# Performance work log

Measured on AMD Instinct MI355X. Metric: run time of the kernel, lower is better.

The kernel has to match this reference:

```python
import jax, jax.numpy as jnp
import numpy as np

B, D, H, W, N = 64, 512, 32, 32, 20
E = 512  # emb_size
TEMP = 10.0


def setup_inputs() -> dict:
    key = jax.random.key(0)
    ks = jax.random.split(key, 16)
    inp = {
        "fvisu": jax.random.normal(ks[0], (B, D, H, W), jnp.float32),
        "fword": jax.random.normal(ks[1], (B, N, D), jnp.float32),
        "context_score": jax.random.uniform(ks[2], (B, N), jnp.float32),
        "fcoord": jax.random.normal(ks[3], (B, 8, H, W), jnp.float32),
        "gest": jax.random.normal(ks[4], (B, 8), jnp.float32),
        "word_mask": jax.random.randint(ks[5], (B, N), 0, 2, jnp.int32),
        # parameters (kaiming-uniform-ish scale)
        "attn_map_w": jax.random.normal(ks[6], (E // 2, D), jnp.float32) * (1.0 / np.sqrt(D)),
        "attn_map_b": jnp.zeros((E // 2,), jnp.float32),
        "attn_score_w": jax.random.normal(ks[7], (1, E // 2), jnp.float32) * (1.0 / np.sqrt(E // 2)),
        "attn_score_b": jnp.zeros((1,), jnp.float32),
        "gamma_w": jax.random.normal(ks[8], (2 * E, D), jnp.float32) * (1.0 / np.sqrt(D)),
        "gamma_b": jnp.zeros((2 * E,), jnp.float32),
        "conv1_w": jax.random.normal(ks[9], (E, D + 8), jnp.float32) * (1.0 / np.sqrt(D + 8)),
        "conv1_b": jnp.zeros((E,), jnp.float32),
    }
    return inp


def mask_softmax(attn_score, word_mask, temp=TEMP):
    # score: (B, N)
    score = jax.nn.softmax(attn_score * temp, axis=1)
    m = word_mask.astype(jnp.int32)
    m = m.at[:, 0].set(0)                      # zero CLS position
    idx = jnp.sum(m, axis=1)                   # index of SEP (post-CLS-zeroing), matches torch loop
    m = m.at[jnp.arange(m.shape[0]), idx].set(0)
    ms = score * m.astype(score.dtype)
    return ms / (jnp.sum(ms, axis=1, keepdims=True) + 1e-8)


def reference(fvisu, fword, context_score, fcoord, gest, word_mask,
              attn_map_w, attn_map_b, attn_score_w, attn_score_b,
              gamma_w, gamma_b, conv1_w, conv1_b):
    # fword: (B, N, D) -> module permutes to (B, D, N)
    fw = jnp.transpose(fword, (0, 2, 1))                      # (B, D, N)
    tile_visu = jnp.mean(fvisu.reshape(B, D, -1), axis=2, keepdims=True)  # (B, D, 1)
    context_tile = tile_visu * fw * context_score[:, None, :]  # (B, D, N)

    # 1x1 Conv1d -> GEMM
    attn_feat = jnp.tanh(jnp.einsum('od,bdn->bon', attn_map_w, context_tile)
                         + attn_map_b[None, :, None])          # (B, E/2, N)
    attn_score = (jnp.einsum('oc,bcn->bon', attn_score_w, attn_feat)[:, 0, :]
                  + attn_score_b[0])                           # (B, N)

    mask_score = mask_softmax(attn_score, word_mask)            # (B, N)
    attn_lang = jnp.einsum('bn,bnd->bd', mask_score, fword)     # (B, D)

    # FiLM parameter decode
    film = attn_lang @ gamma_w.T + gamma_b                      # (B, 2E)
    gammas = jnp.tanh(film[:, :E])[:, :, None, None]
    betas = jnp.tanh(film[:, E:])[:, :, None, None]

    # 1x1 Conv2d on concat(fvisu, fcoord) + InstanceNorm2d (no affine, eps=1e-5)
    x = jnp.concatenate([fvisu, fcoord], axis=1)                # (B, D+8, H, W)
    conv = jnp.einsum('oc,bchw->bohw', conv1_w, x) + conv1_b[None, :, None, None]
    mu = jnp.mean(conv, axis=(2, 3), keepdims=True)
    var = jnp.var(conv, axis=(2, 3), keepdims=True)
    norm = (conv - mu) * jax.lax.rsqrt(var + 1e-5)

    fmodu = jax.nn.relu(gammas * norm + betas)
    fmodu = fvisu + fmodu
    return fmodu, attn_lang, attn_score
```

## Files before the change

kernel.cpp:

```cpp
#include <hip/hip_runtime.h>
#include <math.h>

#define BB 64
#define DD 512
#define HW 1024
#define NN 20
#define EE 512
#define CIN 520
#define KCN 17
#define TEMP_F 10.0f

#define OUT_ALANG (BB*DD*HW)
#define OUT_ASCORE (OUT_ALANG + BB*DD)

typedef __bf16 bf16x8 __attribute__((ext_vector_type(8)));
typedef float f32x4 __attribute__((ext_vector_type(4)));

__device__ __forceinline__ unsigned int pack2bf(float a, float b) {
    unsigned int ua = __builtin_bit_cast(unsigned int, a);
    unsigned int ub = __builtin_bit_cast(unsigned int, b);
    ua += 0x7fffu + ((ua >> 16) & 1u);
    ub += 0x7fffu + ((ub >> 16) & 1u);
    return (ua >> 16) | (ub & 0xffff0000u);
}

__device__ __forceinline__ unsigned short bfr(float x) {
    unsigned int u = __builtin_bit_cast(unsigned int, x);
    u += 0x7fffu + ((u >> 16) & 1u);
    return (unsigned short)(u >> 16);
}

__device__ __forceinline__ float bf2f(unsigned short u) {
    unsigned int x = ((unsigned int)u) << 16;
    return __builtin_bit_cast(float, x);
}

__device__ __forceinline__ void glds16(const void* g, void* l) {
    __builtin_amdgcn_global_load_lds(
        (const __attribute__((address_space(1))) void*)g,
        (__attribute__((address_space(3))) void*)l, 16, 0, 0);
}

__global__ __launch_bounds__(256) void k_tilevisu(const float* __restrict__ fvisu,
                                                  float* __restrict__ tv) {
    int row = blockIdx.x;
    const float4* p = (const float4*)(fvisu + (size_t)row * HW);
    int tid = threadIdx.x;
    float4 v = p[tid];
    float s = v.x + v.y + v.z + v.w;
    #pragma unroll
    for (int off = 32; off; off >>= 1) s += __shfl_down(s, off, 64);
    __shared__ float part[4];
    if ((tid & 63) == 0) part[tid >> 6] = s;
    __syncthreads();
    if (tid == 0) tv[row] = (part[0] + part[1] + part[2] + part[3]) * (1.0f / HW);
}

__global__ __launch_bounds__(512) void k_convert_x(
    const float* __restrict__ fvisu, const float* __restrict__ fcoord,
    unsigned short* __restrict__ Xf, float* __restrict__ tv) {
    int L = blockIdx.x;
    int kc = L % KCN;
    int b  = L / KCN;
    int t = threadIdx.x;
    int co = t >> 7;
    int tl = t & 127;
    int cbase = kc * 32 + co * 8;
    float sums[8];
    #pragma unroll
    for (int j = 0; j < 8; ++j) sums[j] = 0.f;

    #pragma unroll
    for (int i = 0; i < 2; ++i) {
        int p0 = (tl + 128 * i) * 4;
        float4 f4[8];
        #pragma unroll
        for (int j = 0; j < 8; ++j) {
            int c = cbase + j;
            if (c < DD) {
                f4[j] = *(const float4*)&fvisu[((size_t)b * DD + c) * HW + p0];
            } else if (c < CIN) {
                f4[j] = *(const float4*)&fcoord[((size_t)b * 8 + (c - DD)) * HW + p0];
            } else {
                f4[j] = make_float4(0.f, 0.f, 0.f, 0.f);
            }
        }
        #pragma unroll
        for (int j = 0; j < 8; ++j)
            if (cbase + j < DD) sums[j] += f4[j].x + f4[j].y + f4[j].z + f4[j].w;

        size_t base = (((size_t)b * 64 + (p0 >> 4)) * KCN + kc) * 512
                    + (size_t)(co * 16 + (p0 & 15)) * 8;
        #pragma unroll
        for (int i2 = 0; i2 < 4; ++i2) {
            uint4 v;
            v.x = pack2bf(((const float*)&f4[0])[i2], ((const float*)&f4[1])[i2]);
            v.y = pack2bf(((const float*)&f4[2])[i2], ((const float*)&f4[3])[i2]);
            v.z = pack2bf(((const float*)&f4[4])[i2], ((const float*)&f4[5])[i2]);
            v.w = pack2bf(((const float*)&f4[6])[i2], ((const float*)&f4[7])[i2]);
            *(uint4*)&Xf[base + (size_t)i2 * 8] = v;
        }
    }

    #pragma unroll
    for (int j = 0; j < 8; ++j) {
        float s = sums[j];
        #pragma unroll
        for (int off = 32; off; off >>= 1) s += __shfl_down(s, off, 64);
        sums[j] = s;
    }
    __shared__ float red[8][8];
    int w = t >> 6;
    if ((t & 63) == 0) {
        #pragma unroll
        for (int j = 0; j < 8; ++j) red[w][j] = sums[j];
    }
    __syncthreads();
    if (t < 32) {
        int j = t & 7, c2 = t >> 3;
        int c = kc * 32 + c2 * 8 + j;
        if (c < DD) tv[(size_t)b * DD + c] = (red[c2 * 2][j] + red[c2 * 2 + 1][j]) * (1.0f / HW);
    }
}

__global__ __launch_bounds__(256) void k_convert_w(
    const float* __restrict__ cw, unsigned short* __restrict__ Wf) {
    int t = threadIdx.x;
    int frag = blockIdx.x * 4 + (t >> 6);
    int l = t & 63;
    int M = frag / KCN, kc = frag % KCN;
    int o = M * 16 + (l & 15);
    int k0 = kc * 32 + (l >> 4) * 8;
    float f[8];
    #pragma unroll
    for (int j = 0; j < 8; ++j) {
        int k = k0 + j;
        f[j] = (k < CIN) ? cw[(size_t)o * CIN + k] : 0.f;
    }
    uint4 v;
    v.x = pack2bf(f[0], f[1]);
    v.y = pack2bf(f[2], f[3]);
    v.z = pack2bf(f[4], f[5]);
    v.w = pack2bf(f[6], f[7]);
    *(uint4*)&Wf[(size_t)frag * 512 + (size_t)l * 8] = v;
}

__global__ __launch_bounds__(256) void k_convert_w2(
    const float* __restrict__ amw, unsigned short* __restrict__ Whi,
    unsigned short* __restrict__ Wlo) {
    int t = threadIdx.x;
    int fid = blockIdx.x * 4 + (t >> 6);
    int l = t & 63;
    int ot = fid >> 4, ks = fid & 15;
    int o = ot * 16 + (l & 15);
    int k0 = ks * 32 + ((l >> 4) & 3) * 8;
    float hi[8], lo[8];
    #pragma unroll
    for (int j = 0; j < 8; ++j) {
        float x = amw[(size_t)o * DD + k0 + j];
        unsigned short h = bfr(x);
        hi[j] = bf2f(h);
        lo[j] = x - hi[j];
    }
    uint4 vh, vl;
    vh.x = pack2bf(hi[0], hi[1]); vh.y = pack2bf(hi[2], hi[3]);
    vh.z = pack2bf(hi[4], hi[5]); vh.w = pack2bf(hi[6], hi[7]);
    vl.x = pack2bf(lo[0], lo[1]); vl.y = pack2bf(lo[2], lo[3]);
    vl.z = pack2bf(lo[4], lo[5]); vl.w = pack2bf(lo[6], lo[7]);
    *(uint4*)&Whi[(size_t)fid * 512 + (size_t)l * 8] = vh;
    *(uint4*)&Wlo[(size_t)fid * 512 + (size_t)l * 8] = vl;
}

__global__ __launch_bounds__(256) void k_attnscore(
    const float* __restrict__ fword, const float* __restrict__ cs,
    const float* __restrict__ tv, const unsigned short* __restrict__ Whi,
    const unsigned short* __restrict__ Wlo, const float* __restrict__ amb,
    const float* __restrict__ asw, const float* __restrict__ asb,
    float* __restrict__ out_ascore) {
    int b = blockIdx.x;
    __shared__ unsigned short uhi[2][16][64][8];
    __shared__ unsigned short ulo[2][16][64][8];
    __shared__ float scoreP[4][32];
    int t = threadIdx.x;

    {
        int n = t & 31, kq = t >> 5;
        float csv = (n < NN) ? cs[b * NN + n] : 0.f;
        const float* fwp = fword + ((size_t)b * NN + (n < NN ? n : 0)) * DD;
        const float* tvp = tv + (size_t)b * DD;
        int mt = n >> 4;
        #pragma unroll
        for (int oc = 0; oc < 8; ++oc) {
            int k = kq * 64 + oc * 8;
            float x[8];
            if (n < NN) {
                float4 f0 = *(const float4*)&fwp[k];
                float4 f1 = *(const float4*)&fwp[k + 4];
                float4 t0 = *(const float4*)&tvp[k];
                float4 t1 = *(const float4*)&tvp[k + 4];
                x[0] = f0.x * t0.x * csv; x[1] = f0.y * t0.y * csv;
                x[2] = f0.z * t0.z * csv; x[3] = f0.w * t0.w * csv;
                x[4] = f1.x * t1.x * csv; x[5] = f1.y * t1.y * csv;
                x[6] = f1.z * t1.z * csv; x[7] = f1.w * t1.w * csv;
            } else {
                #pragma unroll
                for (int j = 0; j < 8; ++j) x[j] = 0.f;
            }
            float h[8], lw[8];
            #pragma unroll
            for (int j = 0; j < 8; ++j) {
                h[j] = bf2f(bfr(x[j]));
                lw[j] = x[j] - h[j];
            }
            int ks = k >> 5;
            int l = (n & 15) + ((k >> 3) & 3) * 16;
            uint4 vh, vl;
            vh.x = pack2bf(h[0], h[1]); vh.y = pack2bf(h[2], h[3]);
            vh.z = pack2bf(h[4], h[5]); vh.w = pack2bf(h[6], h[7]);
            vl.x = pack2bf(lw[0], lw[1]); vl.y = pack2bf(lw[2], lw[3]);
            vl.z = pack2bf(lw[4], lw[5]); vl.w = pack2bf(lw[6], lw[7]);
            *(uint4*)&uhi[mt][ks][l][0] = vh;
            *(uint4*)&ulo[mt][ks][l][0] = vl;
        }
    }
    __syncthreads();

    int w = t >> 6, l = t & 63;
    f32x4 acc[2][4];
    #pragma unroll
    for (int mt = 0; mt < 2; ++mt)
        #pragma unroll
        for (int nt = 0; nt < 4; ++nt) acc[mt][nt] = (f32x4){0.f, 0.f, 0.f, 0.f};

    #pragma unroll 4
    for (int ks = 0; ks < 16; ++ks) {
        bf16x8 ah0 = *(const bf16x8*)&uhi[0][ks][l][0];
        bf16x8 ah1 = *(const bf16x8*)&uhi[1][ks][l][0];
        bf16x8 al0 = *(const bf16x8*)&ulo[0][ks][l][0];
        bf16x8 al1 = *(const bf16x8*)&ulo[1][ks][l][0];
        #pragma unroll
        for (int nt = 0; nt < 4; ++nt) {
            size_t fo = ((size_t)((w * 4 + nt) * 16 + ks)) * 512 + (size_t)l * 8;
            bf16x8 bh = *(const bf16x8*)&Whi[fo];
            bf16x8 bl = *(const bf16x8*)&Wlo[fo];
            acc[0][nt] = __builtin_amdgcn_mfma_f32_16x16x32_bf16(ah0, bh, acc[0][nt], 0, 0, 0);
            acc[0][nt] = __builtin_amdgcn_mfma_f32_16x16x32_bf16(al0, bh, acc[0][nt], 0, 0, 0);
            acc[0][nt] = __builtin_amdgcn_mfma_f32_16x16x32_bf16(ah0, bl, acc[0][nt], 0, 0, 0);
            acc[1][nt] = __builtin_amdgcn_mfma_f32_16x16x32_bf16(ah1, bh, acc[1][nt], 0, 0, 0);
            acc[1][nt] = __builtin_amdgcn_mfma_f32_16x16x32_bf16(al1, bh, acc[1][nt], 0, 0, 0);
            acc[1][nt] = __builtin_amdgcn_mfma_f32_16x16x32_bf16(ah1, bl, acc[1][nt], 0, 0, 0);
        }
    }

    float ambv[4], aswv[4];
    #pragma unroll
    for (int nt = 0; nt < 4; ++nt) {
        int o = (w * 4 + nt) * 16 + (l & 15);
        ambv[nt] = amb[o];
        aswv[nt] = asw[o];
    }
    #pragma unroll
    for (int mt = 0; mt < 2; ++mt) {
        #pragma unroll
        for (int j = 0; j < 4; ++j) {
            float p = 0.f;
            #pragma unroll
            for (int nt = 0; nt < 4; ++nt)
                p += aswv[nt] * tanhf(acc[mt][nt][j] + ambv[nt]);
            #pragma unroll
            for (int off = 1; off < 16; off <<= 1) p += __shfl_xor(p, off, 64);
            if ((l & 15) == 0) scoreP[w][mt * 16 + (l >> 4) * 4 + j] = p;
        }
    }
    __syncthreads();
    if (t < NN)
        out_ascore[b * NN + t] = scoreP[0][t] + scoreP[1][t] + scoreP[2][t] + scoreP[3][t] + asb[0];
}

__global__ __launch_bounds__(256) void k_attnscore_legacy(
    const float* __restrict__ fword, const float* __restrict__ cs,
    const float* __restrict__ tv, const float* __restrict__ amw,
    const float* __restrict__ amb, const float* __restrict__ asw,
    const float* __restrict__ asb, float* __restrict__ out_ascore) {
    int bn = blockIdx.x;
    int b = bn / NN, n = bn % NN;
    __shared__ float u[DD];
    __shared__ float part[4];
    int tid = threadIdx.x;
    float csv = cs[b * NN + n];
    for (int d = tid; d < DD; d += 256)
        u[d] = tv[b * DD + d] * fword[((size_t)b * NN + n) * DD + d] * csv;
    __syncthreads();
    int o = tid;
    const float4* wrow = (const float4*)(amw + (size_t)o * DD);
    const float4* uv = (const float4*)u;
    float dot = 0.f;
    #pragma unroll 4
    for (int i = 0; i < DD / 4; ++i) {
        float4 w4 = wrow[i]; float4 u4 = uv[i];
        dot += w4.x * u4.x + w4.y * u4.y + w4.z * u4.z + w4.w * u4.w;
    }
    float contrib = asw[o] * tanhf(dot + amb[o]);
    #pragma unroll
    for (int off = 32; off; off >>= 1) contrib += __shfl_down(contrib, off, 64);
    if ((tid & 63) == 0) part[tid >> 6] = contrib;
    __syncthreads();
    if (tid == 0) out_ascore[b * NN + n] = part[0] + part[1] + part[2] + part[3] + asb[0];
}

__global__ __launch_bounds__(256) void k_lang_film(
    const float* __restrict__ fword, const int* __restrict__ wmask,
    const float* __restrict__ ascore, const float* __restrict__ gw,
    const float* __restrict__ gb, float* __restrict__ out_alang,
    float* __restrict__ ws_film) {
    int b = blockIdx.x >> 2;
    int qd = blockIdx.x & 3;
    __shared__ float ms[NN];
    __shared__ float al[DD];
    int tid = threadIdx.x;
    if (tid == 0) {
        float s[NN];
        float mx = -1e30f;
        for (int n = 0; n < NN; ++n) { s[n] = ascore[b * NN + n] * TEMP_F; mx = fmaxf(mx, s[n]); }
        float se = 0.f;
        for (int n = 0; n < NN; ++n) { s[n] = expf(s[n] - mx); se += s[n]; }
        int m[NN]; int idx = 0;
        for (int n = 0; n < NN; ++n) m[n] = wmask[b * NN + n];
        m[0] = 0;
        for (int n = 0; n < NN; ++n) idx += m[n];
        m[idx] = 0;
        float tot = 0.f;
        for (int n = 0; n < NN; ++n) { float v = (s[n] / se) * (float)m[n]; ms[n] = v; tot += v; }
        float inv = 1.f / (tot + 1e-8f);
        for (int n = 0; n < NN; ++n) ms[n] *= inv;
    }
    __syncthreads();
    for (int d = tid; d < DD; d += 256) {
        float a = 0.f;
        #pragma unroll
        for (int n = 0; n < NN; ++n) a += ms[n] * fword[((size_t)b * NN + n) * DD + d];
        al[d] = a;
        if (qd == 0) out_alang[b * DD + d] = a;
    }
    __syncthreads();
    {
        int r = qd * 256 + tid;
        const float4* grow = (const float4*)(gw + (size_t)r * DD);
        const float4* av = (const float4*)al;
        float dot = 0.f;
        #pragma unroll 4
        for (int i = 0; i < DD / 4; ++i) {
            float4 g4 = grow[i]; float4 a4 = av[i];
            dot += g4.x * a4.x + g4.y * a4.y + g4.z * a4.z + g4.w * a4.w;
        }
        ws_film[b * 2 * EE + r] = tanhf(dot + gb[r]);
    }
}

__global__ __launch_bounds__(512, 2) void k_gemm_in_film(
    const unsigned short* __restrict__ Xf, const unsigned short* __restrict__ Wf,
    const float* __restrict__ film, float* __restrict__ out) {
    __shared__ float sP[8][64];
    __shared__ float qP[8][64];
    __shared__ float st[64][4];
    int L = blockIdx.x;
    int r = L & 63, ot = L >> 6;
    int b = ((r >> 3) & 7) * 8 + (r & 7);
    int t = threadIdx.x;
    int w = t >> 6, l = t & 63;

    const unsigned short* Xw = Xf + ((size_t)b * 64 + w * 8) * (KCN * 512) + (size_t)l * 8;
    const unsigned short* Wb = Wf + (size_t)(ot * 4) * (KCN * 512) + (size_t)l * 8;
    int ot2 = 2 * ot;

    f32x4 acc[4][8];
    #pragma unroll
    for (int m = 0; m < 4; ++m)
        #pragma unroll
        for (int n = 0; n < 8; ++n) acc[m][n] = (f32x4){0.f, 0.f, 0.f, 0.f};

    auto kcof = [&](int j) -> int {
        if (j < 15) return j + (j >= ot2 ? 2 : 0);
        return (j == 15) ? ot2 : (ot2 + 1);
    };
    auto loadB = [&](int j, bf16x8* bf_) {
        int kc = kcof(j);
        #pragma unroll
        for (int i = 0; i < 8; ++i)
            bf_[i] = *(const bf16x8*)(Xw + ((size_t)i * KCN + kc) * 512);
    };
    auto loadA = [&](int j, bf16x8* af) {
        int kc = kcof(j);
        #pragma unroll
        for (int m = 0; m < 4; ++m)
            af[m] = *(const bf16x8*)(Wb + ((size_t)m * KCN + kc) * 512);
    };
    auto compute = [&](const bf16x8* af, const bf16x8* bf_) {
        __builtin_amdgcn_s_setprio(1);
        #pragma unroll
        for (int m = 0; m < 4; ++m)
            #pragma unroll
            for (int n = 0; n < 8; ++n)
                acc[m][n] = __builtin_amdgcn_mfma_f32_16x16x32_bf16(af[m], bf_[n], acc[m][n], 0, 0, 0);
        __builtin_amdgcn_s_setprio(0);
    };

    bf16x8 bA[8], bB[8], aA[4], aB[4];
    loadB(0, bA);
    loadA(0, aA);

    #pragma unroll
    for (int j = 0; j < KCN; ++j) {
        if (j & 1) {
            if (j + 1 < KCN) { loadB(j + 1, bA); loadA(j + 1, aA); }
            compute(aB, bB);
        } else {
            if (j + 1 < KCN) { loadB(j + 1, bB); loadA(j + 1, aB); }
            compute(aA, bA);
        }
    }

    #pragma unroll
    for (int m = 0; m < 4; ++m) {
        #pragma unroll
        for (int j = 0; j < 4; ++j) {
            float s = 0.f, q = 0.f;
            #pragma unroll
            for (int n = 0; n < 8; ++n) { float v = acc[m][n][j]; s += v; q += v * v; }
            #pragma unroll
            for (int off = 1; off < 16; off <<= 1) {
                s += __shfl_xor(s, off, 64);
                q += __shfl_xor(q, off, 64);
            }
            if ((l & 15) == 0) {
                int ol = m * 16 + (l >> 4) * 4 + j;
                sP[w][ol] = s;
                qP[w][ol] = q;
            }
        }
    }
    __syncthreads();
    if (t < 64) {
        float s = 0.f, q = 0.f;
        #pragma unroll
        for (int ww = 0; ww < 8; ++ww) { s += sP[ww][t]; q += qP[ww][t]; }
        float mu = s * (1.0f / HW);
        float var = q * (1.0f / HW) - mu * mu;
        int oc = ot * 64 + t;
        st[t][0] = mu;
        st[t][1] = rsqrtf(var + 1e-5f);
        st[t][2] = film[b * 1024 + oc];
        st[t][3] = film[b * 1024 + 512 + oc];
    }
    __syncthreads();

    float* ob = out + ((size_t)b * DD + ot * 64) * HW;
    int q4 = l >> 4;
    #pragma unroll
    for (int m = 0; m < 4; ++m) {
        int kc_m = ot2 + (m >> 1);
        int lp = ((m & 1) * 2 + (q4 >> 1)) * 16 + (l & 15);
        int uo = lp * 8 + (q4 & 1) * 4;
        #pragma unroll
        for (int n = 0; n < 8; ++n) {
            ushort4 rb = *(const ushort4*)(Xf + ((size_t)b * 64 + w * 8 + n) * (KCN * 512)
                                           + ((size_t)kc_m) * 512 + uo);
            int px = w * 128 + n * 16 + (l & 15);
            #pragma unroll
            for (int jj = 0; jj < 4; ++jj) {
                int ol = m * 16 + q4 * 4 + jj;
                f32x4 sv = *(const f32x4*)&st[ol][0];
                float nrm = (acc[m][n][jj] - sv[0]) * sv[1];
                float rr = sv[2] * nrm + sv[3];
                rr = rr > 0.f ? rr : 0.f;
                float res = bf2f(((const unsigned short*)&rb)[jj]);
                ob[(size_t)ol * HW + px] = res + rr;
            }
        }
    }
}

__global__ __launch_bounds__(256) void k_conv_in_film(
    const float* __restrict__ fvisu, const float* __restrict__ fcoord,
    const float* __restrict__ cw, const float* __restrict__ film,
    float* __restrict__ out) {
    int L = blockIdx.x;
    int b = L & 63;
    int tgt = L >> 6;
    int o0 = tgt * 16;
    int tid = threadIdx.x;
    __shared__ float xs[8][HW];
    __shared__ float red[16][4][2];
    __shared__ float stats[16][2];
    float acc[16][4];
    #pragma unroll
    for (int o = 0; o < 16; ++o)
        #pragma unroll
        for (int j = 0; j < 4; ++j) acc[o][j] = 0.f;

    const float* xb_v = fvisu + (size_t)b * DD * HW;
    const float* xb_c = fcoord + (size_t)b * 8 * HW;

    for (int c0 = 0; c0 < CIN; c0 += 8) {
        #pragma unroll
        for (int i = 0; i < 8; ++i) {
            int c = c0 + i;
            const float* src = (c < DD) ? (xb_v + (size_t)c * HW) : (xb_c + (size_t)(c - DD) * HW);
            ((float4*)xs[i])[tid] = ((const float4*)src)[tid];
        }
        __syncthreads();
        #pragma unroll
        for (int i = 0; i < 8; ++i) {
            float xv[4];
            #pragma unroll
            for (int j = 0; j < 4; ++j) xv[j] = xs[i][tid + 256 * j];
            #pragma unroll
            for (int o = 0; o < 16; ++o) {
                float wv = cw[(size_t)(o0 + o) * CIN + (c0 + i)];
                #pragma unroll
                for (int j = 0; j < 4; ++j) acc[o][j] = fmaf(wv, xv[j], acc[o][j]);
            }
        }
        __syncthreads();
    }
    int lane = tid & 63, wid = tid >> 6;
    #pragma unroll
    for (int o = 0; o < 16; ++o) {
        float s = 0.f, q = 0.f;
        #pragma unroll
        for (int j = 0; j < 4; ++j) { s += acc[o][j]; q += acc[o][j] * acc[o][j]; }
        #pragma unroll
        for (int off = 32; off; off >>= 1) {
            s += __shfl_down(s, off, 64);
            q += __shfl_down(q, off, 64);
        }
        if (lane == 0) { red[o][wid][0] = s; red[o][wid][1] = q; }
    }
    __syncthreads();
    if (tid < 16) {
        float s = red[tid][0][0] + red[tid][1][0] + red[tid][2][0] + red[tid][3][0];
        float q = red[tid][0][1] + red[tid][1][1] + red[tid][2][1] + red[tid][3][1];
        float mu = s * (1.0f / HW);
        float var = q * (1.0f / HW) - mu * mu;
        stats[tid][0] = mu;
        stats[tid][1] = rsqrtf(var + 1e-5f);
    }
    __syncthreads();
    #pragma unroll
    for (int o = 0; o < 16; ++o) {
        int oc = o0 + o;
        float mu = stats[o][0], rs = stats[o][1];
        float g  = film[b * 1024 + oc];
        float be = film[b * 1024 + 512 + oc];
        const float* fv = xb_v + (size_t)oc * HW;
        float* op = out + ((size_t)b * DD + oc) * HW;
        #pragma unroll
        for (int j = 0; j < 4; ++j) {
            int p = tid + 256 * j;
            float nrm = (acc[o][j] - mu) * rs;
            float rr = g * nrm + be;
            rr = rr > 0.f ? rr : 0.f;
            op[p] = fv[p] + rr;
        }
    }
}

extern "C" void kernel_launch(void* const* d_in, const int* in_sizes, int n_in,
                              void* d_out, int out_size, void* d_ws, size_t ws_size,
                              hipStream_t stream) {
    const float* fvisu  = (const float*)d_in[0];
    const float* fword  = (const float*)d_in[1];
    const float* cscore = (const float*)d_in[2];
    const float* fcoord = (const float*)d_in[3];
    const int*   wmask  = (const int*)d_in[5];
    const float* amw    = (const float*)d_in[6];
    const float* amb    = (const float*)d_in[7];
    const float* asw    = (const float*)d_in[8];
    const float* asb    = (const float*)d_in[9];
    const float* gw     = (const float*)d_in[10];
    const float* gb     = (const float*)d_in[11];
    const float* cw     = (const float*)d_in[12];

    float* out = (float*)d_out;
    float* ws_tv   = (float*)d_ws;
    float* ws_film = ws_tv + BB * DD;
    unsigned short* Xf  = (unsigned short*)((char*)d_ws + 393216);
    unsigned short* Wf  = (unsigned short*)((char*)d_ws + 393216 + 71303168);
    unsigned short* Whi = (unsigned short*)((char*)d_ws + 393216 + 71303168 + 557056);
    unsigned short* Wlo = Whi + 256 * 512;
    const size_t need = 393216 + 71303168 + 557056 + 524288;

    float* out_alang  = out + OUT_ALANG;
    float* out_ascore = out + OUT_ASCORE;

    if (ws_size >= need) {
        k_convert_w<<<136, 256, 0, stream>>>(cw, Wf);
        k_convert_w2<<<64, 256, 0, stream>>>(amw, Whi, Wlo);
        k_convert_x<<<BB * KCN, 512, 0, stream>>>(fvisu, fcoord, Xf, ws_tv);
        k_attnscore<<<BB, 256, 0, stream>>>(fword, cscore, ws_tv, Whi, Wlo, amb, asw, asb, out_ascore);
        k_lang_film<<<BB * 4, 256, 0, stream>>>(fword, wmask, out_ascore, gw, gb, out_alang, ws_film);
        k_gemm_in_film<<<512, 512, 0, stream>>>(Xf, Wf, ws_film, out);
    } else {
        k_tilevisu<<<BB * DD, 256, 0, stream>>>(fvisu, ws_tv);
        k_attnscore_legacy<<<BB * NN, 256, 0, stream>>>(fword, cscore, ws_tv, amw, amb, asw, asb, out_ascore);
        k_lang_film<<<BB * 4, 256, 0, stream>>>(fword, wmask, out_ascore, gw, gb, out_alang, ws_film);
        k_conv_in_film<<<BB * 32, 256, 0, stream>>>(fvisu, fcoord, cw, ws_film, out);
    }
}
```

Measured before the change: 183.2 us.

## Fuse masked softmax and attn_lang into attnscore; add transposed-weight FiLM kernel

Moves the masked softmax and the attention-weighted sum over words into the tail of the attention-score kernel, so the separate lang/film kernel no longer recomputes them. A new kernel transposes gamma_w into workspace, and a new FiLM kernel computes one batch row per block with coalesced float4 reads of the transposed weights. The block-to-(batch, output tile) mapping in the main GEMM is also changed, altering which blocks share weight tiles in cache. The cost is an extra transpose launch and 2 MB more workspace, and the FiLM GEMV now runs on only 64 blocks.

```diff
diff --git a/kernel.cpp b/kernel.cpp
--- a/kernel.cpp
+++ b/kernel.cpp
@@ -33,12 +33,6 @@
 __device__ __forceinline__ float bf2f(unsigned short u) {
     unsigned int x = ((unsigned int)u) << 16;
     return __builtin_bit_cast(float, x);
-}
-
-__device__ __forceinline__ void glds16(const void* g, void* l) {
-    __builtin_amdgcn_global_load_lds(
-        (const __attribute__((address_space(1))) void*)g,
-        (__attribute__((address_space(3))) void*)l, 16, 0, 0);
 }
 
 __global__ __launch_bounds__(256) void k_tilevisu(const float* __restrict__ fvisu,
@@ -171,16 +165,45 @@
     *(uint4*)&Wlo[(size_t)fid * 512 + (size_t)l * 8] = vl;
 }
 
+__global__ __launch_bounds__(256) void k_convert_gwt(
+    const float* __restrict__ gw, float* __restrict__ gwT) {
+    __shared__ float tile[64][65];
+    int bt = blockIdx.x;
+    int rt = bt & 15, kt = bt >> 4;
+    int t = threadIdx.x;
+    int rl = t >> 4;
+    int kl = (t & 15) * 4;
+    #pragma unroll
+    for (int i = 0; i < 4; ++i) {
+        int rr = rl + i * 16;
+        float4 v = *(const float4*)&gw[(size_t)(rt * 64 + rr) * DD + kt * 64 + kl];
+        tile[rr][kl + 0] = v.x; tile[rr][kl + 1] = v.y;
+        tile[rr][kl + 2] = v.z; tile[rr][kl + 3] = v.w;
+    }
+    __syncthreads();
+    #pragma unroll
+    for (int i = 0; i < 4; ++i) {
+        int kk = rl + i * 16;
+        float4 v;
+        v.x = tile[kl + 0][kk]; v.y = tile[kl + 1][kk];
+        v.z = tile[kl + 2][kk]; v.w = tile[kl + 3][kk];
+        *(float4*)&gwT[(size_t)(kt * 64 + kk) * 1024 + rt * 64 + kl] = v;
+    }
+}
+
 __global__ __launch_bounds__(256) void k_attnscore(
     const float* __restrict__ fword, const float* __restrict__ cs,
     const float* __restrict__ tv, const unsigned short* __restrict__ Whi,
     const unsigned short* __restrict__ Wlo, const float* __restrict__ amb,
     const float* __restrict__ asw, const float* __restrict__ asb,
-    float* __restrict__ out_ascore) {
+    const int* __restrict__ wmask, float* __restrict__ out_ascore,
+    float* __restrict__ out_alang) {
     int b = blockIdx.x;
     __shared__ unsigned short uhi[2][16][64][8];
     __shared__ unsigned short ulo[2][16][64][8];
     __shared__ float scoreP[4][32];
+    __shared__ float asc_sh[NN];
+    __shared__ float msh[NN];
     int t = threadIdx.x;
 
     {
@@ -273,8 +296,38 @@
         }
     }
     __syncthreads();
-    if (t < NN)
-        out_ascore[b * NN + t] = scoreP[0][t] + scoreP[1][t] + scoreP[2][t] + scoreP[3][t] + asb[0];
+    if (t < NN) {
+        float v = scoreP[0][t] + scoreP[1][t] + scoreP[2][t] + scoreP[3][t] + asb[0];
+        out_ascore[b * NN + t] = v;
+        asc_sh[t] = v;
+    }
+    __syncthreads();
+
+    if (t == 0) {
+        float s[NN];
+        float mx = -1e30f;
+        for (int n = 0; n < NN; ++n) { s[n] = asc_sh[n] * TEMP_F; mx = fmaxf(mx, s[n]); }
+        float se = 0.f;
+        for (int n = 0; n < NN; ++n) { s[n] = expf(s[n] - mx); se += s[n]; }
+        int m[NN]; int idx = 0;
+        for (int n = 0; n < NN; ++n) m[n] = wmask[b * NN + n];
+        m[0] = 0;
+        for (int n = 0; n < NN; ++n) idx += m[n];
+        m[idx] = 0;
+        float tot = 0.f;
+        for (int n = 0; n < NN; ++n) { float v = (s[n] / se) * (float)m[n]; msh[n] = v; tot += v; }
+        float inv = 1.f / (tot + 1e-8f);
+        for (int n = 0; n < NN; ++n) msh[n] *= inv;
+    }
+    __syncthreads();
+
+    #pragma unroll 2
+    for (int d = t; d < DD; d += 256) {
+        float a = 0.f;
+        #pragma unroll
+        for (int n = 0; n < NN; ++n) a += msh[n] * fword[((size_t)b * NN + n) * DD + d];
+        out_alang[b * DD + d] = a;
+    }
 }
 
 __global__ __launch_bounds__(256) void k_attnscore_legacy(
@@ -357,6 +410,31 @@
     }
 }
 
+__global__ __launch_bounds__(256) void k_film(
+    const float* __restrict__ alang, const float* __restrict__ gwT,
+    const float* __restrict__ gb, float* __restrict__ ws_film) {
+    int b = blockIdx.x;
+    __shared__ float al[DD];
+    int t = threadIdx.x;
+    al[t] = alang[b * DD + t];
+    al[t + 256] = alang[b * DD + t + 256];
+    __syncthreads();
+    float4 acc = make_float4(0.f, 0.f, 0.f, 0.f);
+    #pragma unroll 8
+    for (int k = 0; k < DD; ++k) {
+        float a = al[k];
+        float4 g = *(const float4*)&gwT[(size_t)k * 1024 + t * 4];
+        acc.x += a * g.x; acc.y += a * g.y; acc.z += a * g.z; acc.w += a * g.w;
+    }
+    float4 gbv = *(const float4*)&gb[t * 4];
+    float4 o;
+    o.x = tanhf(acc.x + gbv.x);
+    o.y = tanhf(acc.y + gbv.y);
+    o.z = tanhf(acc.z + gbv.z);
+    o.w = tanhf(acc.w + gbv.w);
+    *(float4*)&ws_film[b * 1024 + t * 4] = o;
+}
+
 __global__ __launch_bounds__(512, 2) void k_gemm_in_film(
     const unsigned short* __restrict__ Xf, const unsigned short* __restrict__ Wf,
     const float* __restrict__ film, float* __restrict__ out) {
@@ -364,8 +442,8 @@
     __shared__ float qP[8][64];
     __shared__ float st[64][4];
     int L = blockIdx.x;
-    int r = L & 63, ot = L >> 6;
-    int b = ((r >> 3) & 7) * 8 + (r & 7);
+    int ot = (L >> 3) & 7;
+    int b  = (L >> 6) * 8 + (L & 7);
     int t = threadIdx.x;
     int w = t >> 6, l = t & 63;
 
@@ -587,8 +665,9 @@
     unsigned short* Xf  = (unsigned short*)((char*)d_ws + 393216);
     unsigned short* Wf  = (unsigned short*)((char*)d_ws + 393216 + 71303168);
     unsigned short* Whi = (unsigned short*)((char*)d_ws + 393216 + 71303168 + 557056);
-    unsigned short* Wlo = Whi + 256 * 512;
-    const size_t need = 393216 + 71303168 + 557056 + 524288;
+    unsigned short* Wlo = Whi + 131072;
+    float* gwT = (float*)((char*)d_ws + 393216 + 71303168 + 557056 + 524288);
+    const size_t need = 393216 + 71303168 + 557056 + 524288 + 2097152;
 
     float* out_alang  = out + OUT_ALANG;
     float* out_ascore = out + OUT_ASCORE;
@@ -596,9 +675,11 @@
     if (ws_size >= need) {
         k_convert_w<<<136, 256, 0, stream>>>(cw, Wf);
         k_convert_w2<<<64, 256, 0, stream>>>(amw, Whi, Wlo);
+        k_convert_gwt<<<128, 256, 0, stream>>>(gw, gwT);
         k_convert_x<<<BB * KCN, 512, 0, stream>>>(fvisu, fcoord, Xf, ws_tv);
-        k_attnscore<<<BB, 256, 0, stream>>>(fword, cscore, ws_tv, Whi, Wlo, amb, asw, asb, out_ascore);
-        k_lang_film<<<BB * 4, 256, 0, stream>>>(fword, wmask, out_ascore, gw, gb, out_alang, ws_film);
+        k_attnscore<<<BB, 256, 0, stream>>>(fword, cscore, ws_tv, Whi, Wlo, amb, asw, asb,
+                                            wmask, out_ascore, out_alang);
+        k_film<<<BB, 256, 0, stream>>>(out_alang, gwT, gb, ws_film);
         k_gemm_in_film<<<512, 512, 0, stream>>>(Xf, Wf, ws_film, out);
     } else {
         k_tilevisu<<<BB * DD, 256, 0, stream>>>(fvisu, ws_tv);
```

New measurement: 190.6 us. 1.04x slower.
